# Kernel tuning notes

Hardware: AMD Instinct MI355X
Metric: run time of the kernel (lower is better)

Reference implementation:

```python
import jax, jax.numpy as jnp
import numpy as np

N, E, G = 50000, 800000, 128
IN, HID, OUT, H = 128, 64, 32, 4
EPS = 1e-5


def _bn(x, g, b, m, v):
    # BatchNorm1d in eval mode: normalize with running stats
    return (x - m) * jax.lax.rsqrt(v + EPS) * g + b


def _gat(x, src, dst, W, att_src, att_dst, bias, n):
    # PyG GATConv, concat=False: mean over heads
    h = (x @ W).reshape(n, H, -1)                      # [N,H,C]
    a_src = (h * att_src).sum(-1)                      # [N,H]
    a_dst = (h * att_dst).sum(-1)                      # [N,H]
    e = jax.nn.leaky_relu(a_src[src] + a_dst[dst], 0.2)  # [E,H]
    m = jax.ops.segment_max(e, dst, num_segments=n)    # segment softmax over incoming edges
    e = jnp.exp(e - m[dst])
    s = jax.ops.segment_sum(e, dst, num_segments=n)
    alpha = e / s[dst]                                  # [E,H]
    out = jax.ops.segment_sum(alpha[:, :, None] * h[src], dst, num_segments=n)  # [N,H,C]
    return out.mean(axis=1) + bias


def setup_inputs() -> dict:
    key = jax.random.key(0)
    ks = jax.random.split(key, 20)
    d = {
        "x": jax.random.normal(ks[0], (N, IN), jnp.float32),
        "edge_index": jax.random.randint(ks[1], (2, E), 0, N),
        "batch": jnp.sort(jax.random.randint(ks[2], (N,), 0, G)),
        # input_norm
        "in_gamma": jax.random.normal(ks[3], (IN,)) * 0.05 + 1.0,
        "in_beta": jax.random.normal(ks[4], (IN,)) * 0.05,
        "in_mean": jax.random.normal(ks[5], (IN,)) * 0.05,
        "in_var": jax.random.uniform(ks[6], (IN,)) + 0.5,
        # gat1
        "W1": jax.random.normal(ks[7], (IN, H * HID)) * (1.0 / np.sqrt(IN)),
        "as1": jax.random.normal(ks[8], (H, HID)) * 0.1,
        "ad1": jax.random.normal(ks[9], (H, HID)) * 0.1,
        "b1": jnp.zeros((HID,)),
        "bn1_g": jnp.ones((HID,)),
        "bn1_b": jnp.zeros((HID,)),
        "bn1_m": jax.random.normal(ks[10], (HID,)) * 0.05,
        "bn1_v": jax.random.uniform(ks[11], (HID,)) + 0.5,
        # gat2
        "W2": jax.random.normal(ks[12], (HID, H * HID)) * (1.0 / np.sqrt(HID)),
        "as2": jax.random.normal(ks[13], (H, HID)) * 0.1,
        "ad2": jax.random.normal(ks[14], (H, HID)) * 0.1,
        "b2": jnp.zeros((HID,)),
        "bn2_g": jnp.ones((HID,)),
        "bn2_b": jnp.zeros((HID,)),
        "bn2_m": jax.random.normal(ks[15], (HID,)) * 0.05,
        "bn2_v": jax.random.uniform(ks[16], (HID,)) + 0.5,
        # head
        "fc1_w": jax.random.normal(ks[17], (HID, HID // 2)) * (1.0 / np.sqrt(HID)),
        "fc1_b": jnp.zeros((HID // 2,)),
        "fc2_w": jax.random.normal(ks[18], (HID // 2, OUT)) * (1.0 / np.sqrt(HID // 2)),
        "fc2_b": jnp.zeros((OUT,)),
    }
    return d


def reference(x, edge_index, batch, in_gamma, in_beta, in_mean, in_var,
              W1, as1, ad1, b1, bn1_g, bn1_b, bn1_m, bn1_v,
              W2, as2, ad2, b2, bn2_g, bn2_b, bn2_m, bn2_v,
              fc1_w, fc1_b, fc2_w, fc2_b):
    n = x.shape[0]
    # PyG GATConv adds self-loops by default
    loop = jnp.arange(n)
    src = jnp.concatenate([edge_index[0], loop])
    dst = jnp.concatenate([edge_index[1], loop])

    h = _bn(x, in_gamma, in_beta, in_mean, in_var)
    h = _gat(h, src, dst, W1, as1, ad1, b1, n)
    h = jax.nn.relu(_bn(h, bn1_g, bn1_b, bn1_m, bn1_v))
    # dropout p=0.3 is identity in eval mode
    h = _gat(h, src, dst, W2, as2, ad2, b2, n)
    h = jax.nn.relu(_bn(h, bn2_g, bn2_b, bn2_m, bn2_v))

    # global mean pool over graphs
    sums = jax.ops.segment_sum(h, batch, num_segments=G)
    cnts = jax.ops.segment_sum(jnp.ones((n,), h.dtype), batch, num_segments=G)
    emb = sums / jnp.maximum(cnts, 1.0)[:, None]

    out = jax.nn.relu(emb @ fc1_w + fc1_b)
    return out @ fc2_w + fc2_b
```

## Files before the change

kernel.cpp:

```cpp
#include <hip/hip_runtime.h>
#include <hip/hip_bf16.h>

#define EPS   1e-5f
#define NH    4
#define DIN   128
#define DHID  64
#define DOUT  32
#define PNODES 256
#define CAP   128
#define GM    32

typedef __attribute__((ext_vector_type(8))) short short8;
typedef __attribute__((ext_vector_type(4))) float f32x4;
typedef __attribute__((ext_vector_type(2))) float f32x2;

__device__ __forceinline__ float us2f(unsigned short u) {
    return __uint_as_float((unsigned)u << 16);
}
__device__ __forceinline__ unsigned short f2us(float v) {
    __hip_bfloat16 hb = __float2bfloat16(v);
    return *(unsigned short*)&hb;
}
__device__ __forceinline__ unsigned char f2e4m3(float v) {
    int p = __builtin_amdgcn_cvt_pk_fp8_f32(v, 0.f, 0, false);
    return (unsigned char)(p & 0xff);
}
__device__ __forceinline__ float lrelu(float a) { return (a >= 0.f) ? a : 0.2f * a; }

__global__ void k_init0(int* __restrict__ deg, float* __restrict__ pool, int N, int npool) {
    int g = blockIdx.x * blockDim.x + threadIdx.x;
    if (g < N) deg[g] = 1;
    if (g < npool) pool[g] = 0.f;
}

__global__ void k_hist(const int* __restrict__ ei, int* __restrict__ deg, int E) {
    int e = blockIdx.x * blockDim.x + threadIdx.x;
    if (e < E) atomicAdd(&deg[ei[E + e]], 1);
}

__global__ __launch_bounds__(256) void k_scan_a(const int* __restrict__ deg,
                                                int* __restrict__ rowptr,
                                                int* __restrict__ bsum, int N) {
    __shared__ int sh[256];
    const int t = threadIdx.x;
    const int i = blockIdx.x * 256 + t;
    int v = (i < N) ? deg[i] : 0;
    sh[t] = v;
    __syncthreads();
    #pragma unroll
    for (int o = 1; o < 256; o <<= 1) {
        int u = (t >= o) ? sh[t - o] : 0;
        __syncthreads();
        sh[t] += u;
        __syncthreads();
    }
    if (i < N) rowptr[i] = sh[t] - v;
    if (t == 255) bsum[blockIdx.x] = sh[255];
}

__global__ __launch_bounds__(256) void k_scan_b(int* __restrict__ bsum, int nb) {
    __shared__ int sh[256];
    const int t = threadIdx.x;
    int v = (t < nb) ? bsum[t] : 0;
    sh[t] = v;
    __syncthreads();
    #pragma unroll
    for (int o = 1; o < 256; o <<= 1) {
        int u = (t >= o) ? sh[t - o] : 0;
        __syncthreads();
        sh[t] += u;
        __syncthreads();
    }
    if (t < nb) bsum[t] = sh[t] - v;
}

__global__ __launch_bounds__(256) void k_scan_c(int* __restrict__ rowptr,
                                                int* __restrict__ cursor,
                                                const int* __restrict__ bsum,
                                                int N, int Etot) {
    const int i = blockIdx.x * 256 + threadIdx.x;
    if (i < N) {
        int v = rowptr[i] + bsum[blockIdx.x];
        rowptr[i] = v;
        cursor[i] = v;
    }
    if (i == 0) rowptr[N] = Etot;
}

__global__ void k_fill(const int* __restrict__ ei, int* __restrict__ cursor,
                       int* __restrict__ col, int E, int N) {
    int g = blockIdx.x * blockDim.x + threadIdx.x;
    if (g >= E + N) return;
    int s, d;
    if (g < E) { s = ei[g]; d = ei[E + g]; } else { s = d = g - E; }
    int pos = atomicAdd(&cursor[d], 1);
    col[pos] = s;
}

__global__ __launch_bounds__(256) void k_prep(
    const float* __restrict__ x,
    const float* __restrict__ ing, const float* __restrict__ inb,
    const float* __restrict__ inm, const float* __restrict__ inv,
    const float* __restrict__ W1, const float* __restrict__ W2,
    const float* __restrict__ as1, const float* __restrict__ ad1,
    const float* __restrict__ as2, const float* __restrict__ ad2,
    const float* __restrict__ b1,
    const float* __restrict__ bn1g, const float* __restrict__ bn1b,
    const float* __restrict__ bn1m, const float* __restrict__ bn1v,
    unsigned short* __restrict__ A, unsigned short* __restrict__ Wt,
    unsigned short* __restrict__ Wt2,
    unsigned short* __restrict__ Wast1, unsigned short* __restrict__ Wast2,
    float* __restrict__ scl1, float* __restrict__ shf1, int N)
{
    int g = blockIdx.x * blockDim.x + threadIdx.x;
    int totA = N * (DIN / 4);
    if (g < totA) {
        int n = g >> 5, k4 = (g & 31) * 4;
        float4 xv = *(const float4*)(x + (size_t)n * DIN + k4);
        float4 gm = *(const float4*)(ing + k4);
        float4 bb = *(const float4*)(inb + k4);
        float4 mm = *(const float4*)(inm + k4);
        float4 vv = *(const float4*)(inv + k4);
        ushort4 o;
        o.x = f2us((xv.x - mm.x) * rsqrtf(vv.x + EPS) * gm.x + bb.x);
        o.y = f2us((xv.y - mm.y) * rsqrtf(vv.y + EPS) * gm.y + bb.y);
        o.z = f2us((xv.z - mm.z) * rsqrtf(vv.z + EPS) * gm.z + bb.z);
        o.w = f2us((xv.w - mm.w) * rsqrtf(vv.w + EPS) * gm.w + bb.w);
        *(ushort4*)(A + (size_t)n * DIN + k4) = o;
    }
    if (g < 256 * DIN) {
        int n = g >> 7, k = g & 127;
        Wt[g] = f2us(W1[(size_t)k * 256 + n]);
    }
    if (g < 256 * DHID) {
        int n = g >> 6, k = g & 63;
        Wt2[g] = f2us(W2[(size_t)k * 256 + n]);
    }
    if (g < 16 * DIN) {
        int c = g >> 7, k = g & 127;
        float s = 0.f;
        if (c < 4)      { for (int j = 0; j < 64; ++j) s += W1[(size_t)k * 256 + c * 64 + j] * as1[c * 64 + j]; }
        else if (c < 8) { for (int j = 0; j < 64; ++j) s += W1[(size_t)k * 256 + (c - 4) * 64 + j] * ad1[(c - 4) * 64 + j]; }
        Wast1[g] = f2us(s);
    }
    if (g < 16 * DHID) {
        int c = g >> 6, k = g & 63;
        float s = 0.f;
        if (c < 4)      { for (int j = 0; j < 64; ++j) s += W2[(size_t)k * 256 + c * 64 + j] * as2[c * 64 + j]; }
        else if (c < 8) { for (int j = 0; j < 64; ++j) s += W2[(size_t)k * 256 + (c - 4) * 64 + j] * ad2[(c - 4) * 64 + j]; }
        Wast2[g] = f2us(s);
    }
    if (g < DHID) {
        float sc = bn1g[g] * rsqrtf(bn1v[g] + EPS);
        scl1[g] = sc;
        shf1[g] = (b1[g] - bn1m[g]) * sc + bn1b[g];
    }
}

__global__ __launch_bounds__(256) void k_gemm1(
    const unsigned short* __restrict__ A,
    const unsigned short* __restrict__ Wt,
    const unsigned short* __restrict__ Wast,
    unsigned char* __restrict__ h,
    float* __restrict__ asrc, float* __restrict__ adst, int N)
{
    __shared__ float Csh[GM][260];
    const int t = threadIdx.x;
    const int lane = t & 63, wv = t >> 6;
    const int qm = lane & 15, qd = lane >> 4;
    const int base = blockIdx.x * GM;

    short8 afr[2][4];
    #pragma unroll
    for (int rt = 0; rt < 2; ++rt) {
        int node = base + rt * 16 + qm;
        if (node >= N) node = N - 1;
        const unsigned short* ap = A + (size_t)node * DIN + qd * 8;
        #pragma unroll
        for (int ks = 0; ks < 4; ++ks)
            afr[rt][ks] = *(const short8*)(ap + ks * 32);
    }

    const int n0 = wv * 64;
    f32x4 acc[2][4];
    #pragma unroll
    for (int rt = 0; rt < 2; ++rt)
        #pragma unroll
        for (int ct = 0; ct < 4; ++ct)
            acc[rt][ct] = (f32x4){0.f, 0.f, 0.f, 0.f};

    #pragma unroll
    for (int ct = 0; ct < 4; ++ct) {
        const unsigned short* bp = Wt + (size_t)(n0 + ct * 16 + qm) * DIN + qd * 8;
        #pragma unroll
        for (int ks = 0; ks < 4; ++ks) {
            short8 bfr = *(const short8*)(bp + ks * 32);
            acc[0][ct] = __builtin_amdgcn_mfma_f32_16x16x32_bf16(afr[0][ks], bfr, acc[0][ct], 0, 0, 0);
            acc[1][ct] = __builtin_amdgcn_mfma_f32_16x16x32_bf16(afr[1][ks], bfr, acc[1][ct], 0, 0, 0);
        }
    }

    {
        const unsigned short* wp = Wast + (size_t)qm * DIN + qd * 8;
        f32x4 aat[2];
        aat[0] = (f32x4){0.f, 0.f, 0.f, 0.f};
        aat[1] = (f32x4){0.f, 0.f, 0.f, 0.f};
        #pragma unroll
        for (int ks = 0; ks < 4; ++ks) {
            short8 wfr = *(const short8*)(wp + ks * 32);
            aat[0] = __builtin_amdgcn_mfma_f32_16x16x32_bf16(afr[0][ks], wfr, aat[0], 0, 0, 0);
            aat[1] = __builtin_amdgcn_mfma_f32_16x16x32_bf16(afr[1][ks], wfr, aat[1], 0, 0, 0);
        }
        const int c = qm;
        #pragma unroll
        for (int rt = 0; rt < 2; ++rt)
            #pragma unroll
            for (int rg = 0; rg < 4; ++rg) {
                int nd = base + rt * 16 + qd * 4 + rg;
                if (nd < N) {
                    if (c < 4)      asrc[nd * 4 + c] = aat[rt][rg];
                    else if (c < 8) adst[nd * 4 + (c - 4)] = aat[rt][rg];
                }
            }
    }

    #pragma unroll
    for (int rt = 0; rt < 2; ++rt)
        #pragma unroll
        for (int ct = 0; ct < 4; ++ct)
            #pragma unroll
            for (int rg = 0; rg < 4; ++rg)
                Csh[rt * 16 + qd * 4 + rg][n0 + ct * 16 + qm] = acc[rt][ct][rg];
    __syncthreads();

    const int hcol = ((t & 3) << 6) | (t >> 2);
    for (int r = 0; r < GM; ++r) {
        int node = base + r;
        if (node >= N) break;
        h[(size_t)node * 256 + t] = f2e4m3(Csh[r][hcol]);
    }
}

__global__ __launch_bounds__(256) void k_gemm2(
    const unsigned short* __restrict__ A2,
    const unsigned short* __restrict__ Wt2,
    const unsigned short* __restrict__ Wast,
    unsigned char* __restrict__ h,
    float* __restrict__ asrc, float* __restrict__ adst, int N)
{
    __shared__ float Csh[GM][260];
    const int t = threadIdx.x;
    const int lane = t & 63, wv = t >> 6;
    const int qm = lane & 15, qd = lane >> 4;
    const int base = blockIdx.x * GM;

    short8 afr[2][2];
    #pragma unroll
    for (int rt = 0; rt < 2; ++rt) {
        int node = base + rt * 16 + qm;
        if (node >= N) node = N - 1;
        const unsigned short* ap = A2 + (size_t)node * DHID + qd * 8;
        #pragma unroll
        for (int ks = 0; ks < 2; ++ks)
            afr[rt][ks] = *(const short8*)(ap + ks * 32);
    }

    const int n0 = wv * 64;
    f32x4 acc[2][4];
    #pragma unroll
    for (int rt = 0; rt < 2; ++rt)
        #pragma unroll
        for (int ct = 0; ct < 4; ++ct)
            acc[rt][ct] = (f32x4){0.f, 0.f, 0.f, 0.f};

    #pragma unroll
    for (int ct = 0; ct < 4; ++ct) {
        const unsigned short* bp = Wt2 + (size_t)(n0 + ct * 16 + qm) * DHID + qd * 8;
        #pragma unroll
        for (int ks = 0; ks < 2; ++ks) {
            short8 bfr = *(const short8*)(bp + ks * 32);
            acc[0][ct] = __builtin_amdgcn_mfma_f32_16x16x32_bf16(afr[0][ks], bfr, acc[0][ct], 0, 0, 0);
            acc[1][ct] = __builtin_amdgcn_mfma_f32_16x16x32_bf16(afr[1][ks], bfr, acc[1][ct], 0, 0, 0);
        }
    }

    {
        const unsigned short* wp = Wast + (size_t)qm * DHID + qd * 8;
        f32x4 aat[2];
        aat[0] = (f32x4){0.f, 0.f, 0.f, 0.f};
        aat[1] = (f32x4){0.f, 0.f, 0.f, 0.f};
        #pragma unroll
        for (int ks = 0; ks < 2; ++ks) {
            short8 wfr = *(const short8*)(wp + ks * 32);
            aat[0] = __builtin_amdgcn_mfma_f32_16x16x32_bf16(afr[0][ks], wfr, aat[0], 0, 0, 0);
            aat[1] = __builtin_amdgcn_mfma_f32_16x16x32_bf16(afr[1][ks], wfr, aat[1], 0, 0, 0);
        }
        const int c = qm;
        #pragma unroll
        for (int rt = 0; rt < 2; ++rt)
            #pragma unroll
            for (int rg = 0; rg < 4; ++rg) {
                int nd = base + rt * 16 + qd * 4 + rg;
                if (nd < N) {
                    if (c < 4)      asrc[nd * 4 + c] = aat[rt][rg];
                    else if (c < 8) adst[nd * 4 + (c - 4)] = aat[rt][rg];
                }
            }
    }

    #pragma unroll
    for (int rt = 0; rt < 2; ++rt)
        #pragma unroll
        for (int ct = 0; ct < 4; ++ct)
            #pragma unroll
            for (int rg = 0; rg < 4; ++rg)
                Csh[rt * 16 + qd * 4 + rg][n0 + ct * 16 + qm] = acc[rt][ct][rg];
    __syncthreads();

    const int hcol = ((t & 3) << 6) | (t >> 2);
    for (int r = 0; r < GM; ++r) {
        int node = base + r;
        if (node >= N) break;
        h[(size_t)node * 256 + t] = f2e4m3(Csh[r][hcol]);
    }
}

__global__ __launch_bounds__(256) void k_agg(
    const int* __restrict__ rowptr, const int* __restrict__ col,
    const float* __restrict__ asrc, const float* __restrict__ adst,
    const unsigned char* __restrict__ h8,
    float* __restrict__ outf, unsigned short* __restrict__ outb,
    const float* __restrict__ scl, const float* __restrict__ shf,
    int mode, int N)
{
    __shared__ float4 exs[4][CAP];
    __shared__ int    cols[4][CAP];
    const int lane = threadIdx.x & 63;
    const int wv   = threadIdx.x >> 6;
    const int d = (blockIdx.x << 2) + wv;
    if (d >= N) return;
    const int r0  = rowptr[d];
    const int deg = rowptr[d + 1] - r0;

    const float4 ad4 = ((const float4*)adst)[d];
    const float4* __restrict__ as4 = (const float4*)asrc;

    float sm0 = 0.f, sm1 = 0.f, sm2 = 0.f, sm3 = 0.f;
    for (int j = lane; j < deg; j += 64) {
        int s = col[r0 + j];
        float4 a = as4[s];
        float e0 = __expf(lrelu(a.x + ad4.x));
        float e1 = __expf(lrelu(a.y + ad4.y));
        float e2 = __expf(lrelu(a.z + ad4.z));
        float e3 = __expf(lrelu(a.w + ad4.w));
        if (j < CAP) { cols[wv][j] = s; exs[wv][j] = make_float4(e0, e1, e2, e3); }
        sm0 += e0; sm1 += e1; sm2 += e2; sm3 += e3;
    }
    #pragma unroll
    for (int o = 1; o < 64; o <<= 1) {
        sm0 += __shfl_xor(sm0, o, 64);
        sm1 += __shfl_xor(sm1, o, 64);
        sm2 += __shfl_xor(sm2, o, 64);
        sm3 += __shfl_xor(sm3, o, 64);
    }
    const float i0 = 0.25f / sm0, i1 = 0.25f / sm1, i2 = 0.25f / sm2, i3 = 0.25f / sm3;

    const unsigned int* __restrict__ hu = (const unsigned int*)h8;
    float a0 = 0.f, a1 = 0.f, a2 = 0.f, a3 = 0.f;
    float b0 = 0.f, b1 = 0.f, b2 = 0.f, b3 = 0.f;
    if (deg <= CAP) {
        int j = 0;
        for (; j + 3 < deg; j += 4) {
            int sA = cols[wv][j],     sB = cols[wv][j + 1];
            int sC = cols[wv][j + 2], sD = cols[wv][j + 3];
            unsigned int vA = hu[(size_t)sA * 64 + lane];
            unsigned int vB = hu[(size_t)sB * 64 + lane];
            unsigned int vC = hu[(size_t)sC * 64 + lane];
            unsigned int vD = hu[(size_t)sD * 64 + lane];
            float4 wA = exs[wv][j],     wB = exs[wv][j + 1];
            float4 wC = exs[wv][j + 2], wD = exs[wv][j + 3];
            f32x2 lA = __builtin_amdgcn_cvt_pk_f32_fp8(vA, false), hA = __builtin_amdgcn_cvt_pk_f32_fp8(vA, true);
            f32x2 lB = __builtin_amdgcn_cvt_pk_f32_fp8(vB, false), hB = __builtin_amdgcn_cvt_pk_f32_fp8(vB, true);
            f32x2 lC = __builtin_amdgcn_cvt_pk_f32_fp8(vC, false), hC = __builtin_amdgcn_cvt_pk_f32_fp8(vC, true);
            f32x2 lD = __builtin_amdgcn_cvt_pk_f32_fp8(vD, false), hD = __builtin_amdgcn_cvt_pk_f32_fp8(vD, true);
            a0 += wA.x * lA.x; a1 += wA.y * lA.y; a2 += wA.z * hA.x; a3 += wA.w * hA.y;
            b0 += wB.x * lB.x; b1 += wB.y * lB.y; b2 += wB.z * hB.x; b3 += wB.w * hB.y;
            a0 += wC.x * lC.x; a1 += wC.y * lC.y; a2 += wC.z * hC.x; a3 += wC.w * hC.y;
            b0 += wD.x * lD.x; b1 += wD.y * lD.y; b2 += wD.z * hD.x; b3 += wD.w * hD.y;
        }
        for (; j < deg; ++j) {
            int s = cols[wv][j];
            unsigned int v = hu[(size_t)s * 64 + lane];
            float4 w = exs[wv][j];
            f32x2 lo = __builtin_amdgcn_cvt_pk_f32_fp8(v, false), hi = __builtin_amdgcn_cvt_pk_f32_fp8(v, true);
            a0 += w.x * lo.x; a1 += w.y * lo.y; a2 += w.z * hi.x; a3 += w.w * hi.y;
        }
    } else {
        for (int j = 0; j < deg; ++j) {
            int s; float4 w;
            if (j < CAP) { s = cols[wv][j]; w = exs[wv][j]; }
            else {
                s = col[r0 + j];
                float4 a = as4[s];
                w.x = __expf(lrelu(a.x + ad4.x)); w.y = __expf(lrelu(a.y + ad4.y));
                w.z = __expf(lrelu(a.z + ad4.z)); w.w = __expf(lrelu(a.w + ad4.w));
            }
            unsigned int v = hu[(size_t)s * 64 + lane];
            f32x2 lo = __builtin_amdgcn_cvt_pk_f32_fp8(v, false), hi = __builtin_amdgcn_cvt_pk_f32_fp8(v, true);
            a0 += w.x * lo.x; a1 += w.y * lo.y; a2 += w.z * hi.x; a3 += w.w * hi.y;
        }
    }
    float acc = (a0 + b0) * i0 + (a1 + b1) * i1 + (a2 + b2) * i2 + (a3 + b3) * i3;

    if (mode) {
        float v = fmaxf(acc * scl[lane] + shf[lane], 0.f);
        outb[(size_t)d * 64 + lane] = f2us(v);
    } else {
        outf[(size_t)d * 64 + lane] = acc;
    }
}

__global__ __launch_bounds__(256) void k_pool(
    const float* __restrict__ outacc,
    const float* __restrict__ b2_,
    const float* __restrict__ bg, const float* __restrict__ bb,
    const float* __restrict__ bm, const float* __restrict__ bv,
    const int* __restrict__ batch,
    float* __restrict__ pool, float* __restrict__ cnt, int N)
{
    const int lane = threadIdx.x & 63;
    const int wave = threadIdx.x >> 6;
    const int base = blockIdx.x * PNODES;
    int end = base + PNODES; if (end > N) end = N;

    const float scale = bg[lane] * rsqrtf(bv[lane] + EPS);
    const float shift = (b2_[lane] - bm[lane]) * scale + bb[lane];

    float acc = 0.f;
    int cur = -1, cl = 0;
    for (int n = base + wave; n < end; n += 4) {
        int gr = batch[n];
        if (gr != cur) {
            if (cur >= 0) {
                atomicAdd(&pool[cur * 64 + lane], acc);
                if (lane == 0) atomicAdd(&cnt[cur], (float)cl);
            }
            cur = gr; acc = 0.f; cl = 0;
        }
        float v = fmaxf(outacc[(size_t)n * 64 + lane] * scale + shift, 0.f);
        acc += v; ++cl;
    }
    if (cur >= 0) {
        atomicAdd(&pool[cur * 64 + lane], acc);
        if (lane == 0) atomicAdd(&cnt[cur], (float)cl);
    }
}

__global__ void k_head(const float* __restrict__ pool, const float* __restrict__ cnt,
                       const float* __restrict__ fc1w, const float* __restrict__ fc1b,
                       const float* __restrict__ fc2w, const float* __restrict__ fc2b,
                       float* __restrict__ out)
{
    int g = blockIdx.x;
    int t = threadIdx.x;
    __shared__ float emb[64];
    __shared__ float z1[32];
    float c = fmaxf(cnt[g], 1.0f);
    emb[t] = pool[g * 64 + t] / c;
    __syncthreads();
    if (t < 32) {
        float s = fc1b[t];
        for (int k = 0; k < 64; ++k) s += emb[k] * fc1w[k * 32 + t];
        z1[t] = fmaxf(s, 0.f);
    }
    __syncthreads();
    if (t < 32) {
        float o = fc2b[t];
        for (int j = 0; j < 32; ++j) o += z1[j] * fc2w[j * 32 + t];
        out[g * 32 + t] = o;
    }
}

extern "C" void kernel_launch(void* const* d_in, const int* in_sizes, int n_in,
                              void* d_out, int out_size, void* d_ws, size_t ws_size,
                              hipStream_t stream)
{
    const float* x    = (const float*)d_in[0];
    const int*   ei   = (const int*)d_in[1];
    const int*   batch= (const int*)d_in[2];
    const float* ing  = (const float*)d_in[3];
    const float* inb  = (const float*)d_in[4];
    const float* inm  = (const float*)d_in[5];
    const float* inv  = (const float*)d_in[6];
    const float* W1   = (const float*)d_in[7];
    const float* as1  = (const float*)d_in[8];
    const float* ad1  = (const float*)d_in[9];
    const float* b1   = (const float*)d_in[10];
    const float* bn1g = (const float*)d_in[11];
    const float* bn1b = (const float*)d_in[12];
    const float* bn1m = (const float*)d_in[13];
    const float* bn1v = (const float*)d_in[14];
    const float* W2   = (const float*)d_in[15];
    const float* as2  = (const float*)d_in[16];
    const float* ad2  = (const float*)d_in[17];
    const float* b2   = (const float*)d_in[18];
    const float* bn2g = (const float*)d_in[19];
    const float* bn2b = (const float*)d_in[20];
    const float* bn2m = (const float*)d_in[21];
    const float* bn2v = (const float*)d_in[22];
    const float* fc1w = (const float*)d_in[23];
    const float* fc1b = (const float*)d_in[24];
    const float* fc2w = (const float*)d_in[25];
    const float* fc2b = (const float*)d_in[26];

    const int N = in_sizes[0] / DIN;
    const int E = in_sizes[1] / 2;
    const int G = out_size / DOUT;
    const int Etot = E + N;

    unsigned char* h8 = (unsigned char*)d_ws;
    float* asrc   = (float*)(h8 + (size_t)N * 256);
    float* adst   = asrc + (size_t)N * NH;
    unsigned short* Wt    = (unsigned short*)(adst + (size_t)N * NH);
    unsigned short* Wt2   = Wt + 256 * DIN;
    unsigned short* Wast1 = Wt2 + 256 * DHID;
    unsigned short* Wast2 = Wast1 + 16 * DIN;
    float* scl1   = (float*)(Wast2 + 16 * DHID);
    float* shf1   = scl1 + DHID;
    float* outacc = shf1 + DHID;
    unsigned short* A  = (unsigned short*)outacc;
    unsigned short* A2 = (unsigned short*)outacc;
    int*   deg    = (int*)(outacc + (size_t)N * DHID);
    int*   rowptr = deg + N;
    int*   cursor = rowptr + N + 1;
    int*   col    = cursor + N;
    float* pool   = (float*)(col + Etot);
    float* cnt    = pool + (size_t)G * DHID;
    int*   bsum   = (int*)(cnt + G);

    const int npool = G * DHID + G;
    const int nScanBlk = (N + 255) / 256;
    dim3 b256(256);

    k_init0<<<(N + 255) / 256, b256, 0, stream>>>(deg, pool, N, npool);
    k_hist<<<(E + 255) / 256, b256, 0, stream>>>(ei, deg, E);
    k_scan_a<<<nScanBlk, b256, 0, stream>>>(deg, rowptr, bsum, N);
    k_scan_b<<<1, b256, 0, stream>>>(bsum, nScanBlk);
    k_scan_c<<<nScanBlk, b256, 0, stream>>>(rowptr, cursor, bsum, N, Etot);
    k_fill<<<(Etot + 255) / 256, b256, 0, stream>>>(ei, cursor, col, E, N);

    const int prepThreads = N * (DIN / 4);
    k_prep<<<(prepThreads + 255) / 256, b256, 0, stream>>>(
        x, ing, inb, inm, inv, W1, W2, as1, ad1, as2, ad2,
        b1, bn1g, bn1b, bn1m, bn1v,
        A, Wt, Wt2, Wast1, Wast2, scl1, shf1, N);

    k_gemm1<<<(N + GM - 1) / GM, b256, 0, stream>>>(A, Wt, Wast1, h8, asrc, adst, N);
    k_agg<<<(N + 3) / 4, b256, 0, stream>>>(rowptr, col, asrc, adst, h8,
                                            (float*)nullptr, A2, scl1, shf1, 1, N);

    k_gemm2<<<(N + GM - 1) / GM, b256, 0, stream>>>(A2, Wt2, Wast2, h8, asrc, adst, N);
    k_agg<<<(N + 3) / 4, b256, 0, stream>>>(rowptr, col, asrc, adst, h8,
                                            outacc, (unsigned short*)nullptr,
                                            (const float*)nullptr, (const float*)nullptr, 0, N);

    k_pool<<<(N + PNODES - 1) / PNODES, b256, 0, stream>>>(outacc, b2, bn2g, bn2b, bn2m, bn2v,
                                                           batch, pool, cnt, N);
    k_head<<<G, 64, 0, stream>>>(pool, cnt, fc1w, fc1b, fc2w, fc2b, (float*)d_out);
}
```

Before: 374.8 us.

## Bucket edges by destination range before CSR fill to localize atomics

Replaces the direct scatter fill of the CSR column array with a two-pass scheme. Edges are first partitioned into 64 destination-range buckets in an arena, using block-local histograms and one global atomic per bucket per block. A second kernel then fills col bucket by bucket, so cursor atomics and col writes land in a narrower address range. This adds an extra kernel, an extra read and write of all edges as 64-bit pairs, and a fixed-capacity arena that clamps on overflow, which could silently corrupt results on skewed graphs.

```diff
diff --git a/kernel.cpp b/kernel.cpp
--- a/kernel.cpp
+++ b/kernel.cpp
@@ -9,6 +9,8 @@
 #define PNODES 256
 #define CAP   128
 #define GM    32
+#define NBUCK 64
+#define EPB   1024
 
 typedef __attribute__((ext_vector_type(8))) short short8;
 typedef __attribute__((ext_vector_type(4))) float f32x4;
@@ -27,10 +29,12 @@
 }
 __device__ __forceinline__ float lrelu(float a) { return (a >= 0.f) ? a : 0.2f * a; }
 
-__global__ void k_init0(int* __restrict__ deg, float* __restrict__ pool, int N, int npool) {
+__global__ void k_init0(int* __restrict__ deg, float* __restrict__ pool,
+                        int* __restrict__ bcur, int N, int npool) {
     int g = blockIdx.x * blockDim.x + threadIdx.x;
     if (g < N) deg[g] = 1;
     if (g < npool) pool[g] = 0.f;
+    if (g < NBUCK) bcur[g] = 0;
 }
 
 __global__ void k_hist(const int* __restrict__ ei, int* __restrict__ deg, int E) {
@@ -87,12 +91,64 @@
     if (i == 0) rowptr[N] = Etot;
 }
 
-__global__ void k_fill(const int* __restrict__ ei, int* __restrict__ cursor,
-                       int* __restrict__ col, int E, int N) {
-    int g = blockIdx.x * blockDim.x + threadIdx.x;
-    if (g >= E + N) return;
-    int s, d;
-    if (g < E) { s = ei[g]; d = ei[E + g]; } else { s = d = g - E; }
+__global__ __launch_bounds__(256) void k_part(
+    const int* __restrict__ ei, int E, int N, int bshift,
+    unsigned long long* __restrict__ arena, int* __restrict__ bcur, int cap)
+{
+    __shared__ int lhist[NBUCK];
+    __shared__ int lbase[NBUCK];
+    const int t = threadIdx.x;
+    const int e0 = blockIdx.x * EPB;
+    const int eEnd = min(e0 + EPB, E + N);
+
+    if (t < NBUCK) lhist[t] = 0;
+    __syncthreads();
+
+    int myb[4], myd[4], mys[4];
+    #pragma unroll
+    for (int r = 0; r < 4; ++r) {
+        int e = e0 + r * 256 + t;
+        myb[r] = -1;
+        if (e < eEnd) {
+            int s, d;
+            if (e < E) { s = ei[e]; d = ei[E + e]; } else { s = d = e - E; }
+            int b = d >> bshift;
+            myb[r] = b; myd[r] = d; mys[r] = s;
+            atomicAdd(&lhist[b], 1);
+        }
+    }
+    __syncthreads();
+
+    if (t < NBUCK) {
+        int c = lhist[t];
+        lbase[t] = c ? atomicAdd(&bcur[t], c) : 0;
+        lhist[t] = 0;
+    }
+    __syncthreads();
+
+    #pragma unroll
+    for (int r = 0; r < 4; ++r) {
+        int b = myb[r];
+        if (b >= 0) {
+            int li = atomicAdd(&lhist[b], 1);
+            int pos = lbase[b] + li;
+            if (pos >= cap) pos = cap - 1;
+            arena[(size_t)b * cap + pos] =
+                ((unsigned long long)(unsigned)myd[r] << 32) | (unsigned)mys[r];
+        }
+    }
+}
+
+__global__ __launch_bounds__(256) void k_fill2(
+    const unsigned long long* __restrict__ arena, const int* __restrict__ bcnt,
+    int cap, int* __restrict__ cursor, int* __restrict__ col)
+{
+    const int b = blockIdx.x;
+    const int idx = blockIdx.y * 256 + threadIdx.x;
+    if (idx >= bcnt[b]) return;
+    unsigned long long v = arena[(size_t)b * cap + idx];
+    int d = (int)(v >> 32);
+    int s = (int)(v & 0xffffffffu);
     int pos = atomicAdd(&cursor[d], 1);
     col[pos] = s;
 }
@@ -518,6 +574,10 @@
     const int G = out_size / DOUT;
     const int Etot = E + N;
 
+    int bshift = 0;
+    while ((N >> bshift) >= NBUCK) ++bshift;
+    const int cap = (int)(((long long)Etot << bshift) / N * 5 / 4) + 512;
+
     unsigned char* h8 = (unsigned char*)d_ws;
     float* asrc   = (float*)(h8 + (size_t)N * 256);
     float* adst   = asrc + (size_t)N * NH;
@@ -537,17 +597,24 @@
     float* pool   = (float*)(col + Etot);
     float* cnt    = pool + (size_t)G * DHID;
     int*   bsum   = (int*)(cnt + G);
+    int*   bcur   = bsum + 256;
+    unsigned long long* arena =
+        (unsigned long long*)(((size_t)(bcur + NBUCK) + 7) & ~(size_t)7);
 
     const int npool = G * DHID + G;
     const int nScanBlk = (N + 255) / 256;
     dim3 b256(256);
 
-    k_init0<<<(N + 255) / 256, b256, 0, stream>>>(deg, pool, N, npool);
+    k_init0<<<(N + 255) / 256, b256, 0, stream>>>(deg, pool, bcur, N, npool);
     k_hist<<<(E + 255) / 256, b256, 0, stream>>>(ei, deg, E);
     k_scan_a<<<nScanBlk, b256, 0, stream>>>(deg, rowptr, bsum, N);
     k_scan_b<<<1, b256, 0, stream>>>(bsum, nScanBlk);
     k_scan_c<<<nScanBlk, b256, 0, stream>>>(rowptr, cursor, bsum, N, Etot);
-    k_fill<<<(Etot + 255) / 256, b256, 0, stream>>>(ei, cursor, col, E, N);
+    k_part<<<(Etot + EPB - 1) / EPB, b256, 0, stream>>>(ei, E, N, bshift, arena, bcur, cap);
+    {
+        dim3 gFill(NBUCK, (cap + 255) / 256);
+        k_fill2<<<gFill, b256, 0, stream>>>(arena, bcur, cap, cursor, col);
+    }
 
     const int prepThreads = N * (DIN / 4);
     k_prep<<<(prepThreads + 255) / 256, b256, 0, stream>>>(
```

Result: no change. 373.1 us (-0.5%).
